# Kernel tuning notes

Measured on AMD Instinct MI355X. Metric: run time of the kernel, lower is better.

The kernel has to match this reference:

```python
import jax, jax.numpy as jnp
import numpy as np

N_NODES = 50000

def _gat_conv(x, src, dst, W, a_src, a_dst, bias, num_nodes, concat, neg_slope=0.2):
    # x: [N, Fin]; W: [Fin, H*C]; a_src/a_dst: [H, C]; src/dst: [E]
    H, C = a_src.shape
    h = (x @ W).reshape(-1, H, C)                      # [N, H, C]
    alpha_s = jnp.einsum('nhc,hc->nh', h, a_src)        # [N, H]
    alpha_d = jnp.einsum('nhc,hc->nh', h, a_dst)        # [N, H]
    e = alpha_s[src] + alpha_d[dst]                     # [E, H]
    e = jax.nn.leaky_relu(e, neg_slope)
    # segment softmax over destination nodes
    m = jax.ops.segment_max(e, dst, num_segments=num_nodes)   # [N, H]
    ex = jnp.exp(e - m[dst])                                   # [E, H]
    denom = jax.ops.segment_sum(ex, dst, num_segments=num_nodes)  # [N, H]
    alpha = ex / denom[dst]                                    # [E, H]
    msg = h[src] * alpha[:, :, None]                            # [E, H, C]
    out = jax.ops.segment_sum(msg, dst, num_segments=num_nodes)  # [N, H, C]
    if concat:
        out = out.reshape(-1, H * C)
    else:
        out = out.mean(axis=1)
    return out + bias

def _add_self_loops(edge_index, num_nodes):
    loop = jnp.arange(num_nodes, dtype=edge_index.dtype)
    src = jnp.concatenate([edge_index[0], loop])
    dst = jnp.concatenate([edge_index[1], loop])
    return src, dst

def setup_inputs() -> dict:
    key = jax.random.key(0)
    ks = jax.random.split(key, 12)
    N, E = N_NODES, 800000
    in_c, hid, out_c, H = 128, 32, 64, 4
    x = jax.random.normal(ks[0], (N, in_c), dtype=jnp.float32)
    edge_index = jax.random.randint(ks[1], (2, E), 0, N, dtype=jnp.int64)
    edge_weight = jax.random.uniform(ks[2], (E,), dtype=jnp.float32)
    s1 = 1.0 / np.sqrt(in_c)
    s2 = 1.0 / np.sqrt(hid * H)
    W1 = jax.random.normal(ks[3], (in_c, H * hid), dtype=jnp.float32) * s1
    a_src1 = jax.random.normal(ks[4], (H, hid), dtype=jnp.float32) * s1
    a_dst1 = jax.random.normal(ks[5], (H, hid), dtype=jnp.float32) * s1
    b1 = jnp.zeros((H * hid,), dtype=jnp.float32)
    W2 = jax.random.normal(ks[6], (H * hid, out_c), dtype=jnp.float32) * s2
    a_src2 = jax.random.normal(ks[7], (1, out_c), dtype=jnp.float32) * s2
    a_dst2 = jax.random.normal(ks[8], (1, out_c), dtype=jnp.float32) * s2
    b2 = jnp.zeros((out_c,), dtype=jnp.float32)
    return {"x": x, "edge_index": edge_index, "edge_weight": edge_weight,
            "W1": W1, "a_src1": a_src1, "a_dst1": a_dst1, "b1": b1,
            "W2": W2, "a_src2": a_src2, "a_dst2": a_dst2, "b2": b2}

def reference(x, edge_index, edge_weight, W1, a_src1, a_dst1, b1, W2, a_src2, a_dst2, b2):
    # PyG GATConv with edge_dim unset ignores edge_weight; self-loops added by default
    N = x.shape[0]
    src, dst = _add_self_loops(edge_index, N)
    h = _gat_conv(x, src, dst, W1, a_src1, a_dst1, b1, N, concat=True)
    h = jax.nn.relu(h)
    out = _gat_conv(h, src, dst, W2, a_src2, a_dst2, b2, N, concat=False)
    return out
```

## Files before the change

kernel.cpp:

```cpp
#include <hip/hip_runtime.h>
#include <hip/hip_fp16.h>
#include <math.h>


#define NEG_SLOPE 0.2f
#define NBLKA 256
#define MAXNB 512
#define LDH 136

typedef _Float16 f16x8 __attribute__((ext_vector_type(8)));
typedef float f32x4 __attribute__((ext_vector_type(4)));

__device__ __forceinline__ float leaky(float v) { return v > 0.f ? v : NEG_SLOPE * v; }

__global__ __launch_bounds__(256) void histc_k(const int* __restrict__ ei, int E, int ET,
                                               int* __restrict__ blkpref, int NB,
                                               const float* __restrict__ W1,
                                               const float* __restrict__ W2,
                                               _Float16* __restrict__ w1t,
                                               _Float16* __restrict__ w2t) {
  __shared__ int lhist[MAXNB];
  int chunk = (ET + NBLKA - 1) / NBLKA;
  int e0 = blockIdx.x * chunk, e1 = min(ET, e0 + chunk);
  for (int b = threadIdx.x; b < NB; b += 256) lhist[b] = 0;
  __syncthreads();
  for (int e = e0 + threadIdx.x; e < e1; e += 256) {
    int d = (e < E) ? ei[E + e] : (e - E);
    atomicAdd(&lhist[d >> 7], 1);
  }
  __syncthreads();
  for (int b = threadIdx.x; b < NB; b += 256)
    blkpref[b * NBLKA + blockIdx.x] = lhist[b];
  if (blockIdx.x == 0) {
    int t = threadIdx.x;
    if (t < 128) {
      union { _Float16 h[8]; uint4 u; } buf;
      for (int k0 = 0; k0 < 128; k0 += 8) {
        #pragma unroll
        for (int u = 0; u < 8; ++u) buf.h[u] = (_Float16)W1[(k0 + u) * 128 + t];
        *(uint4*)&w1t[t * 128 + k0] = buf.u;
      }
    } else if (t < 192) {
      int n = t - 128;
      union { _Float16 h[8]; uint4 u; } buf;
      for (int k0 = 0; k0 < 128; k0 += 8) {
        #pragma unroll
        for (int u = 0; u < 8; ++u) buf.h[u] = (_Float16)W2[(k0 + u) * 64 + n];
        *(uint4*)&w2t[n * 128 + k0] = buf.u;
      }
    }
  }
}

__global__ __launch_bounds__(256) void scan_blk_k(int* __restrict__ blkpref,
                                                  int* __restrict__ bbase) {
  __shared__ int sm[NBLKA];
  int b = blockIdx.x, t = threadIdx.x;
  int v = blkpref[b * NBLKA + t];
  sm[t] = v;
  __syncthreads();
  #pragma unroll
  for (int off = 1; off < NBLKA; off <<= 1) {
    int x = (t >= off) ? sm[t - off] : 0;
    __syncthreads();
    sm[t] += x;
    __syncthreads();
  }
  blkpref[b * NBLKA + t] = sm[t] - v;
  if (t == NBLKA - 1) bbase[b] = sm[t];
}

__global__ __launch_bounds__(512) void scan_bkt_k(int* __restrict__ bbase,
                                                  int* __restrict__ lcnt,
                                                  int* __restrict__ rowptr,
                                                  int NB, int N, int ET) {
  __shared__ int sm[512];
  int t = threadIdx.x;
  int v = (t < NB) ? bbase[t] : 0;
  sm[t] = v;
  __syncthreads();
  #pragma unroll
  for (int off = 1; off < 512; off <<= 1) {
    int x = (t >= off) ? sm[t - off] : 0;
    __syncthreads();
    sm[t] += x;
    __syncthreads();
  }
  int excl = sm[t] - v;
  if (t <= NB) bbase[t] = excl;
  if (t == 0) { lcnt[0] = 0; lcnt[16] = 0; rowptr[N] = ET; }
}

__global__ __launch_bounds__(256) void passA_k(const int* __restrict__ ei, int E, int ET,
                                               const int* __restrict__ bbase,
                                               const int* __restrict__ blkpref,
                                               int* __restrict__ pairs, int NB) {
  __shared__ int lcur[MAXNB];
  int chunk = (ET + NBLKA - 1) / NBLKA;
  int e0 = blockIdx.x * chunk, e1 = min(ET, e0 + chunk);
  for (int b = threadIdx.x; b < NB; b += 256)
    lcur[b] = bbase[b] + blkpref[b * NBLKA + blockIdx.x];
  __syncthreads();
  for (int e = e0 + threadIdx.x; e < e1; e += 256) {
    int s, d;
    if (e < E) { s = ei[e]; d = ei[E + e]; } else { s = d = e - E; }
    int b = d >> 7;
    int pos = atomicAdd(&lcur[b], 1);
    pairs[pos] = ((d & 127) << 17) | s;
  }
}

__global__ __launch_bounds__(256) void passB_k(const int* __restrict__ pairs,
                                               const int* __restrict__ bbase,
                                               int* __restrict__ rowptr,
                                               int* __restrict__ srcs,
                                               int* __restrict__ small_list,
                                               int* __restrict__ big_list,
                                               int* __restrict__ lcnt, int N) {
  __shared__ int ncnt[128], spre[128], lcur[128];
  __shared__ int wcS[2], wcB[2], bS, bB;
  int b = blockIdx.x, t = threadIdx.x;
  int nb0 = b << 7;
  int nn = min(128, N - nb0);
  int e0 = bbase[b], e1 = bbase[b + 1];
  if (t < 128) ncnt[t] = 0;
  __syncthreads();
  for (int r = e0 + t; r < e1; r += 256)
    atomicAdd(&ncnt[pairs[r] >> 17], 1);
  __syncthreads();
  if (t < 128) spre[t] = ncnt[t];
  __syncthreads();
  #pragma unroll
  for (int off = 1; off < 128; off <<= 1) {
    int x = (t < 128 && t >= off) ? spre[t - off] : 0;
    __syncthreads();
    if (t < 128) spre[t] += x;
    __syncthreads();
  }
  if (t < nn) {
    int base = e0 + spre[t] - ncnt[t];
    rowptr[nb0 + t] = base;
    lcur[t] = base;
  }
  __syncthreads();
  for (int r = e0 + t; r < e1; r += 256) {
    int p = pairs[r];
    int pos = atomicAdd(&lcur[p >> 17], 1);
    srcs[pos] = p & 0x1FFFF;
  }
  int lane = t & 63, wv = t >> 6;
  bool valid = (t < nn);
  int deg = valid ? ncnt[t] : 0;
  bool isS = valid && (deg <= 16);
  bool isB = valid && (deg > 16);
  unsigned long long ms = __ballot(isS);
  unsigned long long mb = __ballot(isB);
  if (lane == 0 && wv < 2) { wcS[wv] = __popcll(ms); wcB[wv] = __popcll(mb); }
  __syncthreads();
  if (t == 0) {
    bS = atomicAdd(&lcnt[0],  wcS[0] + wcS[1]);
    bB = atomicAdd(&lcnt[16], wcB[0] + wcB[1]);
  }
  __syncthreads();
  unsigned long long below = (lane == 0) ? 0ull : (~0ull >> (64 - lane));
  int offS = bS + ((wv == 1) ? wcS[0] : 0);
  int offB = bB + ((wv == 1) ? wcB[0] : 0);
  if (isS) small_list[offS + __popcll(ms & below)] = nb0 + t;
  if (isB) big_list[offB + __popcll(mb & below)]   = nb0 + t;
}

__global__ __launch_bounds__(256) void gemm1_k(const float* __restrict__ X,
                                               const _Float16* __restrict__ WT,
                                               const float* __restrict__ aw_s,
                                               const float* __restrict__ aw_d,
                                               __half* __restrict__ Hh,
                                               float* __restrict__ as,
                                               float* __restrict__ ad, int N) {
  __shared__ _Float16 xs[64 * LDH];
  __shared__ _Float16 wt[128 * LDH];
  int t = threadIdx.x;
  int n0 = blockIdx.x * 64;
  for (int i = t; i < 2048; i += 256) {
    int r = i >> 4, c8 = i & 15;
    *(uint4*)&wt[r * LDH + c8 * 8] = ((const uint4*)WT)[i];
  }
  for (int i = t; i < 2048; i += 256) {
    int r = i >> 5, c4 = i & 31;
    int n = n0 + r;
    float4 xv = (n < N) ? ((const float4*)X)[(size_t)n * 32 + c4]
                        : make_float4(0.f, 0.f, 0.f, 0.f);
    __half2 h0 = __floats2half2_rn(xv.x, xv.y);
    __half2 h1 = __floats2half2_rn(xv.z, xv.w);
    uint2 u; u.x = *(unsigned*)&h0; u.y = *(unsigned*)&h1;
    *(uint2*)&xs[r * LDH + c4 * 4] = u;
  }
  __syncthreads();
  int wv = t >> 6, l = t & 63;
  int row16 = l & 15, kg = l >> 4;
  f32x4 acc[8];
  #pragma unroll
  for (int j = 0; j < 8; ++j) acc[j] = (f32x4){0.f, 0.f, 0.f, 0.f};
  #pragma unroll
  for (int kk = 0; kk < 4; ++kk) {
    int kbase = kk * 32 + kg * 8;
    f16x8 afr = *(f16x8*)&xs[(wv * 16 + row16) * LDH + kbase];
    #pragma unroll
    for (int j = 0; j < 8; ++j) {
      f16x8 bfr = *(f16x8*)&wt[(j * 16 + row16) * LDH + kbase];
      acc[j] = __builtin_amdgcn_mfma_f32_16x16x32_f16(afr, bfr, acc[j], 0, 0, 0);
    }
  }
  __syncthreads();
  #pragma unroll
  for (int j = 0; j < 8; ++j) {
    int col = j * 16 + row16;
    #pragma unroll
    for (int r = 0; r < 4; ++r) {
      int row = wv * 16 + kg * 4 + r;
      xs[row * LDH + col] = (_Float16)acc[j][r];
    }
  }
  __syncthreads();
  for (int i = t; i < 1024; i += 256) {
    int r = i >> 4, c8 = i & 15;
    int n = n0 + r;
    if (n < N) ((uint4*)Hh)[(size_t)n * 16 + c8] = *(uint4*)&xs[r * LDH + c8 * 8];
  }
  {
    int r = t >> 2, h = t & 3;
    int n = n0 + r;
    float ps = 0.f, pd = 0.f;
    #pragma unroll
    for (int q = 0; q < 4; ++q) {
      f16x8 hv = *(f16x8*)&xs[r * LDH + h * 32 + q * 8];
      float4 s0 = *(const float4*)&aw_s[h * 32 + q * 8];
      float4 s1 = *(const float4*)&aw_s[h * 32 + q * 8 + 4];
      float4 d0 = *(const float4*)&aw_d[h * 32 + q * 8];
      float4 d1 = *(const float4*)&aw_d[h * 32 + q * 8 + 4];
      ps += (float)hv[0] * s0.x + (float)hv[1] * s0.y + (float)hv[2] * s0.z + (float)hv[3] * s0.w
          + (float)hv[4] * s1.x + (float)hv[5] * s1.y + (float)hv[6] * s1.z + (float)hv[7] * s1.w;
      pd += (float)hv[0] * d0.x + (float)hv[1] * d0.y + (float)hv[2] * d0.z + (float)hv[3] * d0.w
          + (float)hv[4] * d1.x + (float)hv[5] * d1.y + (float)hv[6] * d1.z + (float)hv[7] * d1.w;
    }
    if (n < N) { as[n * 4 + h] = ps; ad[n * 4 + h] = pd; }
  }
}

__global__ __launch_bounds__(256) void gemm2_k(const __half* __restrict__ X,
                                               const _Float16* __restrict__ WT,
                                               const float* __restrict__ aw_s,
                                               const float* __restrict__ aw_d,
                                               __half* __restrict__ Hh,
                                               float* __restrict__ as,
                                               float* __restrict__ ad, int N) {
  __shared__ _Float16 xs[64 * LDH];
  __shared__ _Float16 wt[64 * LDH];
  int t = threadIdx.x;
  int n0 = blockIdx.x * 64;
  for (int i = t; i < 1024; i += 256) {
    int r = i >> 4, c8 = i & 15;
    *(uint4*)&wt[r * LDH + c8 * 8] = ((const uint4*)WT)[i];
  }
  for (int i = t; i < 1024; i += 256) {
    int r = i >> 4, c8 = i & 15;
    int n = n0 + r;
    uint4 v = (n < N) ? ((const uint4*)X)[(size_t)n * 16 + c8] : make_uint4(0, 0, 0, 0);
    *(uint4*)&xs[r * LDH + c8 * 8] = v;
  }
  __syncthreads();
  int wv = t >> 6, l = t & 63;
  int row16 = l & 15, kg = l >> 4;
  f32x4 acc[4];
  #pragma unroll
  for (int j = 0; j < 4; ++j) acc[j] = (f32x4){0.f, 0.f, 0.f, 0.f};
  #pragma unroll
  for (int kk = 0; kk < 4; ++kk) {
    int kbase = kk * 32 + kg * 8;
    f16x8 afr = *(f16x8*)&xs[(wv * 16 + row16) * LDH + kbase];
    #pragma unroll
    for (int j = 0; j < 4; ++j) {
      f16x8 bfr = *(f16x8*)&wt[(j * 16 + row16) * LDH + kbase];
      acc[j] = __builtin_amdgcn_mfma_f32_16x16x32_f16(afr, bfr, acc[j], 0, 0, 0);
    }
  }
  __syncthreads();
  #pragma unroll
  for (int j = 0; j < 4; ++j) {
    int col = j * 16 + row16;
    #pragma unroll
    for (int r = 0; r < 4; ++r) {
      int row = wv * 16 + kg * 4 + r;
      xs[row * LDH + col] = (_Float16)acc[j][r];
    }
  }
  __syncthreads();
  for (int i = t; i < 512; i += 256) {
    int r = i >> 3, c8 = i & 7;
    int n = n0 + r;
    if (n < N) ((uint4*)Hh)[(size_t)n * 8 + c8] = *(uint4*)&xs[r * LDH + c8 * 8];
  }
  {
    int r = t >> 2, q = t & 3;
    int n = n0 + r;
    float ps = 0.f, pd = 0.f;
    #pragma unroll
    for (int qq = 0; qq < 2; ++qq) {
      f16x8 hv = *(f16x8*)&xs[r * LDH + q * 16 + qq * 8];
      float4 s0 = *(const float4*)&aw_s[q * 16 + qq * 8];
      float4 s1 = *(const float4*)&aw_s[q * 16 + qq * 8 + 4];
      float4 d0 = *(const float4*)&aw_d[q * 16 + qq * 8];
      float4 d1 = *(const float4*)&aw_d[q * 16 + qq * 8 + 4];
      ps += (float)hv[0] * s0.x + (float)hv[1] * s0.y + (float)hv[2] * s0.z + (float)hv[3] * s0.w
          + (float)hv[4] * s1.x + (float)hv[5] * s1.y + (float)hv[6] * s1.z + (float)hv[7] * s1.w;
      pd += (float)hv[0] * d0.x + (float)hv[1] * d0.y + (float)hv[2] * d0.z + (float)hv[3] * d0.w
          + (float)hv[4] * d1.x + (float)hv[5] * d1.y + (float)hv[6] * d1.z + (float)hv[7] * d1.w;
    }
    ps += __shfl_xor(ps, 1); ps += __shfl_xor(ps, 2);
    pd += __shfl_xor(pd, 1); pd += __shfl_xor(pd, 2);
    if (q == 0 && n < N) { as[n] = ps; ad[n] = pd; }
  }
}

__device__ __forceinline__ void load8h(const __half* p, float* f) {
  uint4 hv = *(const uint4*)p;
  float2 f0 = __half22float2(*(const __half2*)&hv.x);
  float2 f1 = __half22float2(*(const __half2*)&hv.y);
  float2 f2 = __half22float2(*(const __half2*)&hv.z);
  float2 f3 = __half22float2(*(const __half2*)&hv.w);
  f[0] = f0.x; f[1] = f0.y; f[2] = f1.x; f[3] = f1.y;
  f[4] = f2.x; f[5] = f2.y; f[6] = f3.x; f[7] = f3.y;
}

__global__ __launch_bounds__(256) void agg1_k(const int* __restrict__ rowptr,
                                              const int* __restrict__ srcs,
                                              const float* __restrict__ as,
                                              const float* __restrict__ ad,
                                              const __half* __restrict__ Hm,
                                              const float* __restrict__ bias,
                                              __half* __restrict__ out,
                                              const int* __restrict__ small_list,
                                              const int* __restrict__ big_list,
                                              const int* __restrict__ lcnt, int SB) {
  if (blockIdx.x < (unsigned)SB) {
    __shared__ float al_sm[16][17][4];
    __shared__ int   sr_sm[16][16];
    int g  = threadIdx.x >> 4;
    int gl = threadIdx.x & 15;
    int gidx = blockIdx.x * 16 + g;
    if (gidx >= lcnt[0]) return;
    int n = small_list[gidx];
    int r0 = rowptr[n];
    int deg = rowptr[n + 1] - r0;
    float4 adn = *(const float4*)&ad[n * 4];

    float e0 = -INFINITY, e1 = -INFINITY, e2 = -INFINITY, e3 = -INFINITY;
    int s = 0;
    if (gl < deg) {
      s = srcs[r0 + gl];
      float4 av = *(const float4*)&as[s * 4];
      e0 = leaky(av.x + adn.x); e1 = leaky(av.y + adn.y);
      e2 = leaky(av.z + adn.z); e3 = leaky(av.w + adn.w);
    }
    sr_sm[g][gl] = s;
    float m0 = e0, m1 = e1, m2 = e2, m3 = e3;
    #pragma unroll
    for (int off = 8; off > 0; off >>= 1) {
      m0 = fmaxf(m0, __shfl_xor(m0, off, 16)); m1 = fmaxf(m1, __shfl_xor(m1, off, 16));
      m2 = fmaxf(m2, __shfl_xor(m2, off, 16)); m3 = fmaxf(m3, __shfl_xor(m3, off, 16));
    }
    float sc0 = (gl < deg) ? __expf(e0 - m0) : 0.f;
    float sc1 = (gl < deg) ? __expf(e1 - m1) : 0.f;
    float sc2 = (gl < deg) ? __expf(e2 - m2) : 0.f;
    float sc3 = (gl < deg) ? __expf(e3 - m3) : 0.f;
    float s0 = sc0, s1 = sc1, s2 = sc2, s3 = sc3;
    #pragma unroll
    for (int off = 8; off > 0; off >>= 1) {
      s0 += __shfl_xor(s0, off, 16); s1 += __shfl_xor(s1, off, 16);
      s2 += __shfl_xor(s2, off, 16); s3 += __shfl_xor(s3, off, 16);
    }
    *(float4*)&al_sm[g][gl][0] =
        make_float4(sc0 / s0, sc1 / s1, sc2 / s2, sc3 / s3);

    int h = gl >> 2;
    int cbase = gl * 8;
    float a0 = 0.f, a1 = 0.f, a2 = 0.f, a3 = 0.f,
          a4 = 0.f, a5 = 0.f, a6 = 0.f, a7 = 0.f;
    for (int j = 0; j < deg; j += 4) {
      #pragma unroll
      for (int u = 0; u < 4; ++u) {
        int idx = j + u;
        bool vU = idx < deg;
        int jj = vU ? idx : 0;
        int   sU  = sr_sm[g][jj];
        float alU = vU ? al_sm[g][jj][h] : 0.f;
        float f[8];
        load8h(&Hm[(size_t)sU * 128 + cbase], f);
        a0 += f[0] * alU; a1 += f[1] * alU; a2 += f[2] * alU; a3 += f[3] * alU;
        a4 += f[4] * alU; a5 += f[5] * alU; a6 += f[6] * alU; a7 += f[7] * alU;
      }
    }
    float4 b0 = *(const float4*)&bias[cbase];
    float4 b1 = *(const float4*)&bias[cbase + 4];
    __half2* dst = (__half2*)&out[(size_t)n * 128 + cbase];
    dst[0] = __floats2half2_rn(fmaxf(a0 + b0.x, 0.f), fmaxf(a1 + b0.y, 0.f));
    dst[1] = __floats2half2_rn(fmaxf(a2 + b0.z, 0.f), fmaxf(a3 + b0.w, 0.f));
    dst[2] = __floats2half2_rn(fmaxf(a4 + b1.x, 0.f), fmaxf(a5 + b1.y, 0.f));
    dst[3] = __floats2half2_rn(fmaxf(a6 + b1.z, 0.f), fmaxf(a7 + b1.w, 0.f));
    return;
  }
  __shared__ float al_sm[4][64][4];
  __shared__ int   sr_sm[4][64];
  int wv = threadIdx.x >> 6, lane = threadIdx.x & 63;
  int widx = (blockIdx.x - SB) * 4 + wv;
  if (widx >= lcnt[16]) return;
  int n = big_list[widx];
  int r0 = rowptr[n], r1 = rowptr[n + 1];
  int deg = r1 - r0;
  int grp = lane >> 4, gl = lane & 15, h = gl >> 2;
  int cbase = gl * 8;
  float4 adn = *(const float4*)&ad[n * 4];

  float a0 = 0.f, a1 = 0.f, a2 = 0.f, a3 = 0.f,
        a4 = 0.f, a5 = 0.f, a6 = 0.f, a7 = 0.f;

  if (deg <= 64) {
    float e0 = -INFINITY, e1 = -INFINITY, e2 = -INFINITY, e3 = -INFINITY;
    int s = 0;
    if (lane < deg) {
      s = srcs[r0 + lane];
      float4 av = *(const float4*)&as[s * 4];
      e0 = leaky(av.x + adn.x); e1 = leaky(av.y + adn.y);
      e2 = leaky(av.z + adn.z); e3 = leaky(av.w + adn.w);
    }
    sr_sm[wv][lane] = s;
    float m0 = e0, m1 = e1, m2 = e2, m3 = e3;
    #pragma unroll
    for (int off = 32; off > 0; off >>= 1) {
      m0 = fmaxf(m0, __shfl_xor(m0, off)); m1 = fmaxf(m1, __shfl_xor(m1, off));
      m2 = fmaxf(m2, __shfl_xor(m2, off)); m3 = fmaxf(m3, __shfl_xor(m3, off));
    }
    float sc0 = (lane < deg) ? __expf(e0 - m0) : 0.f;
    float sc1 = (lane < deg) ? __expf(e1 - m1) : 0.f;
    float sc2 = (lane < deg) ? __expf(e2 - m2) : 0.f;
    float sc3 = (lane < deg) ? __expf(e3 - m3) : 0.f;
    float s0 = sc0, s1 = sc1, s2 = sc2, s3 = sc3;
    #pragma unroll
    for (int off = 32; off > 0; off >>= 1) {
      s0 += __shfl_xor(s0, off); s1 += __shfl_xor(s1, off);
      s2 += __shfl_xor(s2, off); s3 += __shfl_xor(s3, off);
    }
    *(float4*)&al_sm[wv][lane][0] =
        make_float4(sc0 / s0, sc1 / s1, sc2 / s2, sc3 / s3);

    for (int base = 0; base < deg; base += 16) {
      #pragma unroll
      for (int u = 0; u < 4; ++u) {
        int idx = base + grp * 4 + u;
        bool vU = idx < deg;
        int jj = vU ? idx : 0;
        int   sU  = sr_sm[wv][jj];
        float alU = vU ? al_sm[wv][jj][h] : 0.f;
        float f[8];
        load8h(&Hm[(size_t)sU * 128 + cbase], f);
        a0 += f[0] * alU; a1 += f[1] * alU; a2 += f[2] * alU; a3 += f[3] * alU;
        a4 += f[4] * alU; a5 += f[5] * alU; a6 += f[6] * alU; a7 += f[7] * alU;
      }
    }
  } else {
    float m0 = -INFINITY, m1 = -INFINITY, m2 = -INFINITY, m3 = -INFINITY;
    for (int r = r0 + lane; r < r1; r += 64) {
      int s = srcs[r];
      float4 av = *(const float4*)&as[s * 4];
      m0 = fmaxf(m0, leaky(av.x + adn.x)); m1 = fmaxf(m1, leaky(av.y + adn.y));
      m2 = fmaxf(m2, leaky(av.z + adn.z)); m3 = fmaxf(m3, leaky(av.w + adn.w));
    }
    #pragma unroll
    for (int off = 32; off > 0; off >>= 1) {
      m0 = fmaxf(m0, __shfl_xor(m0, off)); m1 = fmaxf(m1, __shfl_xor(m1, off));
      m2 = fmaxf(m2, __shfl_xor(m2, off)); m3 = fmaxf(m3, __shfl_xor(m3, off));
    }
    float s0 = 0.f, s1 = 0.f, s2 = 0.f, s3 = 0.f;
    for (int r = r0 + lane; r < r1; r += 64) {
      int s = srcs[r];
      float4 av = *(const float4*)&as[s * 4];
      s0 += __expf(leaky(av.x + adn.x) - m0); s1 += __expf(leaky(av.y + adn.y) - m1);
      s2 += __expf(leaky(av.z + adn.z) - m2); s3 += __expf(leaky(av.w + adn.w) - m3);
    }
    #pragma unroll
    for (int off = 32; off > 0; off >>= 1) {
      s0 += __shfl_xor(s0, off); s1 += __shfl_xor(s1, off);
      s2 += __shfl_xor(s2, off); s3 += __shfl_xor(s3, off);
    }
    float mhh = (h == 0) ? m0 : (h == 1) ? m1 : (h == 2) ? m2 : m3;
    float inv = 1.f / ((h == 0) ? s0 : (h == 1) ? s1 : (h == 2) ? s2 : s3);
    float adh = (h == 0) ? adn.x : (h == 1) ? adn.y : (h == 2) ? adn.z : adn.w;
    for (int r = r0; r < r1; r += 8) {
      int rA = r + grp, rB = rA + 4;
      bool vA = rA < r1, vB = rB < r1;
      int sA = srcs[vA ? rA : r0];
      int sB = srcs[vB ? rB : r0];
      float avA = as[sA * 4 + h], avB = as[sB * 4 + h];
      float alA = vA ? (__expf(leaky(avA + adh) - mhh) * inv) : 0.f;
      float alB = vB ? (__expf(leaky(avB + adh) - mhh) * inv) : 0.f;
      float fA[8], fB[8];
      load8h(&Hm[(size_t)sA * 128 + cbase], fA);
      load8h(&Hm[(size_t)sB * 128 + cbase], fB);
      a0 += fA[0] * alA + fB[0] * alB; a1 += fA[1] * alA + fB[1] * alB;
      a2 += fA[2] * alA + fB[2] * alB; a3 += fA[3] * alA + fB[3] * alB;
      a4 += fA[4] * alA + fB[4] * alB; a5 += fA[5] * alA + fB[5] * alB;
      a6 += fA[6] * alA + fB[6] * alB; a7 += fA[7] * alA + fB[7] * alB;
    }
  }
  a0 += __shfl_xor(a0, 16); a0 += __shfl_xor(a0, 32);
  a1 += __shfl_xor(a1, 16); a1 += __shfl_xor(a1, 32);
  a2 += __shfl_xor(a2, 16); a2 += __shfl_xor(a2, 32);
  a3 += __shfl_xor(a3, 16); a3 += __shfl_xor(a3, 32);
  a4 += __shfl_xor(a4, 16); a4 += __shfl_xor(a4, 32);
  a5 += __shfl_xor(a5, 16); a5 += __shfl_xor(a5, 32);
  a6 += __shfl_xor(a6, 16); a6 += __shfl_xor(a6, 32);
  a7 += __shfl_xor(a7, 16); a7 += __shfl_xor(a7, 32);
  if (grp == 0) {
    float4 b0 = *(const float4*)&bias[cbase];
    float4 b1 = *(const float4*)&bias[cbase + 4];
    __half2* dst = (__half2*)&out[(size_t)n * 128 + cbase];
    dst[0] = __floats2half2_rn(fmaxf(a0 + b0.x, 0.f), fmaxf(a1 + b0.y, 0.f));
    dst[1] = __floats2half2_rn(fmaxf(a2 + b0.z, 0.f), fmaxf(a3 + b0.w, 0.f));
    dst[2] = __floats2half2_rn(fmaxf(a4 + b1.x, 0.f), fmaxf(a5 + b1.y, 0.f));
    dst[3] = __floats2half2_rn(fmaxf(a6 + b1.z, 0.f), fmaxf(a7 + b1.w, 0.f));
  }
}

__global__ __launch_bounds__(256) void agg2_k(const int* __restrict__ rowptr,
                                              const int* __restrict__ srcs,
                                              const float* __restrict__ as,
                                              const float* __restrict__ ad,
                                              const __half* __restrict__ Hm,
                                              const float* __restrict__ bias,
                                              float* __restrict__ out,
                                              const int* __restrict__ small_list,
                                              const int* __restrict__ big_list,
                                              const int* __restrict__ lcnt, int SB) {
  if (blockIdx.x < (unsigned)SB) {
    __shared__ float al_sm[16][17];
    __shared__ int   sr_sm[16][16];
    int g  = threadIdx.x >> 4;
    int gl = threadIdx.x & 15;
    int gidx = blockIdx.x * 16 + g;
    if (gidx >= lcnt[0]) return;
    int n = small_list[gidx];
    int r0 = rowptr[n];
    int deg = rowptr[n + 1] - r0;
    float adn = ad[n];

    float e = -INFINITY;
    int s = 0;
    if (gl < deg) { s = srcs[r0 + gl]; e = leaky(as[s] + adn); }
    sr_sm[g][gl] = s;
    float m = e;
    #pragma unroll
    for (int off = 8; off > 0; off >>= 1) m = fmaxf(m, __shfl_xor(m, off, 16));
    float sc = (gl < deg) ? __expf(e - m) : 0.f;
    float ssum = sc;
    #pragma unroll
    for (int off = 8; off > 0; off >>= 1) ssum += __shfl_xor(ssum, off, 16);
    al_sm[g][gl] = sc / ssum;

    int cbase = gl * 4;
    float a0 = 0.f, a1 = 0.f, a2 = 0.f, a3 = 0.f;
    for (int j = 0; j < deg; j += 4) {
      #pragma unroll
      for (int u = 0; u < 4; ++u) {
        int idx = j + u;
        bool vU = idx < deg;
        int jj = vU ? idx : 0;
        int   sU  = sr_sm[g][jj];
        float alU = vU ? al_sm[g][jj] : 0.f;
        uint2 hv = *(const uint2*)&Hm[(size_t)sU * 64 + cbase];
        float2 f0 = __half22float2(*(const __half2*)&hv.x);
        float2 f1 = __half22float2(*(const __half2*)&hv.y);
        a0 += f0.x * alU; a1 += f0.y * alU; a2 += f1.x * alU; a3 += f1.y * alU;
      }
    }
    float4 bv = *(const float4*)&bias[cbase];
    float4 o;
    o.x = a0 + bv.x; o.y = a1 + bv.y; o.z = a2 + bv.z; o.w = a3 + bv.w;
    *(float4*)&out[(size_t)n * 64 + cbase] = o;
    return;
  }
  __shared__ float al_sm[4][64];
  __shared__ int   sr_sm[4][64];
  int wv = threadIdx.x >> 6, lane = threadIdx.x & 63;
  int widx = (blockIdx.x - SB) * 4 + wv;
  if (widx >= lcnt[16]) return;
  int n = big_list[widx];
  int r0 = rowptr[n], r1 = rowptr[n + 1];
  int deg = r1 - r0;
  int grp = lane >> 4, gl = lane & 15;
  int cbase = gl * 4;
  float adn = ad[n];

  float a0 = 0.f, a1 = 0.f, a2 = 0.f, a3 = 0.f;

  if (deg <= 64) {
    float e = -INFINITY;
    int s = 0;
    if (lane < deg) { s = srcs[r0 + lane]; e = leaky(as[s] + adn); }
    sr_sm[wv][lane] = s;
    float m = e;
    #pragma unroll
    for (int off = 32; off > 0; off >>= 1) m = fmaxf(m, __shfl_xor(m, off));
    float sc = (lane < deg) ? __expf(e - m) : 0.f;
    float ssum = sc;
    #pragma unroll
    for (int off = 32; off > 0; off >>= 1) ssum += __shfl_xor(ssum, off);
    al_sm[wv][lane] = sc / ssum;

    for (int base = 0; base < deg; base += 16) {
      #pragma unroll
      for (int u = 0; u < 4; ++u) {
        int idx = base + grp * 4 + u;
        bool vU = idx < deg;
        int jj = vU ? idx : 0;
        int   sU  = sr_sm[wv][jj];
        float alU = vU ? al_sm[wv][jj] : 0.f;
        uint2 hv = *(const uint2*)&Hm[(size_t)sU * 64 + cbase];
        float2 f0 = __half22float2(*(const __half2*)&hv.x);
        float2 f1 = __half22float2(*(const __half2*)&hv.y);
        a0 += f0.x * alU; a1 += f0.y * alU; a2 += f1.x * alU; a3 += f1.y * alU;
      }
    }
  } else {
    float mh = -INFINITY;
    for (int r = r0 + lane; r < r1; r += 64)
      mh = fmaxf(mh, leaky(as[srcs[r]] + adn));
    #pragma unroll
    for (int off = 32; off > 0; off >>= 1) mh = fmaxf(mh, __shfl_xor(mh, off));
    float ssum = 0.f;
    for (int r = r0 + lane; r < r1; r += 64)
      ssum += __expf(leaky(as[srcs[r]] + adn) - mh);
    #pragma unroll
    for (int off = 32; off > 0; off >>= 1) ssum += __shfl_xor(ssum, off);
    float inv = 1.f / ssum;
    for (int r = r0; r < r1; r += 8) {
      int rA = r + grp, rB = rA + 4;
      bool vA = rA < r1, vB = rB < r1;
      int sA = srcs[vA ? rA : r0];
      int sB = srcs[vB ? rB : r0];
      float alA = vA ? (__expf(leaky(as[sA] + adn) - mh) * inv) : 0.f;
      float alB = vB ? (__expf(leaky(as[sB] + adn) - mh) * inv) : 0.f;
      uint2 hvA = *(const uint2*)&Hm[(size_t)sA * 64 + cbase];
      uint2 hvB = *(const uint2*)&Hm[(size_t)sB * 64 + cbase];
      float2 fA0 = __half22float2(*(const __half2*)&hvA.x);
      float2 fA1 = __half22float2(*(const __half2*)&hvA.y);
      float2 fB0 = __half22float2(*(const __half2*)&hvB.x);
      float2 fB1 = __half22float2(*(const __half2*)&hvB.y);
      a0 += fA0.x * alA + fB0.x * alB; a1 += fA0.y * alA + fB0.y * alB;
      a2 += fA1.x * alA + fB1.x * alB; a3 += fA1.y * alA + fB1.y * alB;
    }
  }
  a0 += __shfl_xor(a0, 16); a0 += __shfl_xor(a0, 32);
  a1 += __shfl_xor(a1, 16); a1 += __shfl_xor(a1, 32);
  a2 += __shfl_xor(a2, 16); a2 += __shfl_xor(a2, 32);
  a3 += __shfl_xor(a3, 16); a3 += __shfl_xor(a3, 32);
  if (grp == 0) {
    float4 bv = *(const float4*)&bias[cbase];
    float4 o;
    o.x = a0 + bv.x; o.y = a1 + bv.y; o.z = a2 + bv.z; o.w = a3 + bv.w;
    *(float4*)&out[(size_t)n * 64 + cbase] = o;
  }
}

extern "C" void kernel_launch(void* const* d_in, const int* in_sizes, int n_in,
                              void* d_out, int out_size, void* d_ws, size_t ws_size,
                              hipStream_t stream) {
  const float* x   = (const float*)d_in[0];
  const int*   ei  = (const int*)d_in[1];
  const float* W1  = (const float*)d_in[3];
  const float* aS1 = (const float*)d_in[4];
  const float* aD1 = (const float*)d_in[5];
  const float* b1  = (const float*)d_in[6];
  const float* W2  = (const float*)d_in[7];
  const float* aS2 = (const float*)d_in[8];
  const float* aD2 = (const float*)d_in[9];
  const float* b2  = (const float*)d_in[10];

  const int N  = in_sizes[0] / 128;
  const int E  = in_sizes[2];
  const int ET = E + N;
  const int NB = (N + 127) >> 7;

  float* ws    = (float*)d_ws;
  __half* h1h  = (__half*)ws;
  __half* o1h  = (__half*)(ws + (size_t)N * 64);
  float* as1   = ws + (size_t)N * 128;
  float* ad1   = as1  + (size_t)4 * N;
  float* as2   = ad1  + (size_t)4 * N;
  float* ad2   = as2  + (size_t)N;
  int*   lcnt    = (int*)(ad2 + (size_t)N);
  int*   rowptr  = lcnt + 32;
  int*   bbase   = rowptr + N + 1;
  int*   blkpref = bbase + NB + 1;
  int*   small_list = blkpref + NB * NBLKA;
  int*   big_list   = small_list + N;
  int*   srcs   = big_list + N;
  _Float16* w1t = (_Float16*)(srcs + ET);
  _Float16* w2t = w1t + 128 * 128;
  int*   pairs  = (int*)ws;
  __half* h2h  = h1h;
  float* out  = (float*)d_out;

  const int gb = (N + 63) / 64;
  const int sb = (N + 15) / 16;
  const int bb = (N + 3) / 4;

  histc_k<<<NBLKA, 256, 0, stream>>>(ei, E, ET, blkpref, NB, W1, W2, w1t, w2t);
  scan_blk_k<<<NB, 256, 0, stream>>>(blkpref, bbase);
  scan_bkt_k<<<1, 512, 0, stream>>>(bbase, lcnt, rowptr, NB, N, ET);
  passA_k<<<NBLKA, 256, 0, stream>>>(ei, E, ET, bbase, blkpref, pairs, NB);
  passB_k<<<NB, 256, 0, stream>>>(pairs, bbase, rowptr, srcs,
                                  small_list, big_list, lcnt, N);

  gemm1_k<<<gb, 256, 0, stream>>>(x, w1t, aS1, aD1, h1h, as1, ad1, N);
  agg1_k<<<sb + bb, 256, 0, stream>>>(rowptr, srcs, as1, ad1, h1h, b1, o1h,
                                      small_list, big_list, lcnt, sb);

  gemm2_k<<<gb, 256, 0, stream>>>(o1h, w2t, aS2, aD2, h2h, as2, ad2, N);
  agg2_k<<<sb + bb, 256, 0, stream>>>(rowptr, srcs, as2, ad2, h2h, b2, out,
                                      small_list, big_list, lcnt, sb);
}
```

Baseline: 216.4 us.

## Fuse layer-1 GEMM into histogram kernel via block-index dispatch

```diff
diff --git a/kernel.cpp b/kernel.cpp
--- a/kernel.cpp
+++ b/kernel.cpp
@@ -10,45 +10,116 @@
 
 typedef _Float16 f16x8 __attribute__((ext_vector_type(8)));
 typedef float f32x4 __attribute__((ext_vector_type(4)));
+typedef unsigned int u32x4 __attribute__((ext_vector_type(4)));
 
 __device__ __forceinline__ float leaky(float v) { return v > 0.f ? v : NEG_SLOPE * v; }
 
-__global__ __launch_bounds__(256) void histc_k(const int* __restrict__ ei, int E, int ET,
-                                               int* __restrict__ blkpref, int NB,
-                                               const float* __restrict__ W1,
-                                               const float* __restrict__ W2,
-                                               _Float16* __restrict__ w1t,
-                                               _Float16* __restrict__ w2t) {
-  __shared__ int lhist[MAXNB];
-  int chunk = (ET + NBLKA - 1) / NBLKA;
-  int e0 = blockIdx.x * chunk, e1 = min(ET, e0 + chunk);
-  for (int b = threadIdx.x; b < NB; b += 256) lhist[b] = 0;
-  __syncthreads();
-  for (int e = e0 + threadIdx.x; e < e1; e += 256) {
-    int d = (e < E) ? ei[E + e] : (e - E);
-    atomicAdd(&lhist[d >> 7], 1);
-  }
-  __syncthreads();
-  for (int b = threadIdx.x; b < NB; b += 256)
-    blkpref[b * NBLKA + blockIdx.x] = lhist[b];
-  if (blockIdx.x == 0) {
-    int t = threadIdx.x;
-    if (t < 128) {
-      union { _Float16 h[8]; uint4 u; } buf;
+__global__ __launch_bounds__(256) void histc_gemm1_k(const int* __restrict__ ei, int E, int ET,
+                                                     int* __restrict__ blkpref, int NB,
+                                                     const float* __restrict__ W1,
+                                                     const float* __restrict__ W2,
+                                                     _Float16* __restrict__ w2t,
+                                                     const float* __restrict__ X,
+                                                     const float* __restrict__ aw_s,
+                                                     const float* __restrict__ aw_d,
+                                                     __half* __restrict__ Hh,
+                                                     float* __restrict__ as,
+                                                     float* __restrict__ ad, int N) {
+  __shared__ float smemf[13056];
+  int t = threadIdx.x;
+  if (blockIdx.x < NBLKA) {
+    int* lhist = (int*)smemf;
+    int chunk = (ET + NBLKA - 1) / NBLKA;
+    int e0 = blockIdx.x * chunk, e1 = min(ET, e0 + chunk);
+    for (int b = t; b < NB; b += 256) lhist[b] = 0;
+    __syncthreads();
+    for (int e = e0 + t; e < e1; e += 256) {
+      int d = (e < E) ? ei[E + e] : (e - E);
+      atomicAdd(&lhist[d >> 7], 1);
+    }
+    __syncthreads();
+    for (int b = t; b < NB; b += 256)
+      blkpref[b * NBLKA + blockIdx.x] = lhist[b];
+    if (blockIdx.x == 0 && t < 64) {
+      union { _Float16 h[8]; u32x4 u; } buf;
       for (int k0 = 0; k0 < 128; k0 += 8) {
         #pragma unroll
-        for (int u = 0; u < 8; ++u) buf.h[u] = (_Float16)W1[(k0 + u) * 128 + t];
-        *(uint4*)&w1t[t * 128 + k0] = buf.u;
+        for (int u = 0; u < 8; ++u) buf.h[u] = (_Float16)W2[(k0 + u) * 64 + t];
+        *(u32x4*)&w2t[t * 128 + k0] = buf.u;
       }
-    } else if (t < 192) {
-      int n = t - 128;
-      union { _Float16 h[8]; uint4 u; } buf;
-      for (int k0 = 0; k0 < 128; k0 += 8) {
-        #pragma unroll
-        for (int u = 0; u < 8; ++u) buf.h[u] = (_Float16)W2[(k0 + u) * 64 + n];
-        *(uint4*)&w2t[n * 128 + k0] = buf.u;
-      }
-    }
+    }
+    return;
+  }
+  _Float16* xs = (_Float16*)smemf;
+  _Float16* wt = xs + 64 * LDH;
+  int n0 = (blockIdx.x - NBLKA) * 64;
+  for (int i = t; i < 4096; i += 256) {
+    int k = i >> 5, n4 = (i & 31) * 4;
+    float4 wv = *(const float4*)&W1[k * 128 + n4];
+    wt[(n4 + 0) * LDH + k] = (_Float16)wv.x;
+    wt[(n4 + 1) * LDH + k] = (_Float16)wv.y;
+    wt[(n4 + 2) * LDH + k] = (_Float16)wv.z;
+    wt[(n4 + 3) * LDH + k] = (_Float16)wv.w;
+  }
+  for (int i = t; i < 2048; i += 256) {
+    int r = i >> 5, c4 = i & 31;
+    int n = n0 + r;
+    float4 xv = (n < N) ? *(const float4*)&X[(size_t)n * 128 + c4 * 4]
+                        : make_float4(0.f, 0.f, 0.f, 0.f);
+    __half2 h0 = __floats2half2_rn(xv.x, xv.y);
+    __half2 h1 = __floats2half2_rn(xv.z, xv.w);
+    uint2 u; u.x = *(unsigned*)&h0; u.y = *(unsigned*)&h1;
+    *(uint2*)&xs[r * LDH + c4 * 4] = u;
+  }
+  __syncthreads();
+  int wv = t >> 6, l = t & 63;
+  int row16 = l & 15, kg = l >> 4;
+  f32x4 acc[8];
+  #pragma unroll
+  for (int j = 0; j < 8; ++j) acc[j] = (f32x4){0.f, 0.f, 0.f, 0.f};
+  #pragma unroll
+  for (int kk = 0; kk < 4; ++kk) {
+    int kbase = kk * 32 + kg * 8;
+    f16x8 afr = *(f16x8*)&xs[(wv * 16 + row16) * LDH + kbase];
+    #pragma unroll
+    for (int j = 0; j < 8; ++j) {
+      f16x8 bfr = *(f16x8*)&wt[(j * 16 + row16) * LDH + kbase];
+      acc[j] = __builtin_amdgcn_mfma_f32_16x16x32_f16(afr, bfr, acc[j], 0, 0, 0);
+    }
+  }
+  __syncthreads();
+  #pragma unroll
+  for (int j = 0; j < 8; ++j) {
+    int col = j * 16 + row16;
+    #pragma unroll
+    for (int r = 0; r < 4; ++r) {
+      int row = wv * 16 + kg * 4 + r;
+      xs[row * LDH + col] = (_Float16)acc[j][r];
+    }
+  }
+  __syncthreads();
+  for (int i = t; i < 1024; i += 256) {
+    int r = i >> 4, c8 = i & 15;
+    int n = n0 + r;
+    if (n < N) ((u32x4*)Hh)[(size_t)n * 16 + c8] = *(u32x4*)&xs[r * LDH + c8 * 8];
+  }
+  {
+    int r = t >> 2, h = t & 3;
+    int n = n0 + r;
+    float ps = 0.f, pd = 0.f;
+    #pragma unroll
+    for (int q = 0; q < 4; ++q) {
+      f16x8 hv = *(f16x8*)&xs[r * LDH + h * 32 + q * 8];
+      float4 s0 = *(const float4*)&aw_s[h * 32 + q * 8];
+      float4 s1 = *(const float4*)&aw_s[h * 32 + q * 8 + 4];
+      float4 d0 = *(const float4*)&aw_d[h * 32 + q * 8];
+      float4 d1 = *(const float4*)&aw_d[h * 32 + q * 8 + 4];
+      ps += (float)hv[0] * s0.x + (float)hv[1] * s0.y + (float)hv[2] * s0.z + (float)hv[3] * s0.w
+          + (float)hv[4] * s1.x + (float)hv[5] * s1.y + (float)hv[6] * s1.z + (float)hv[7] * s1.w;
+      pd += (float)hv[0] * d0.x + (float)hv[1] * d0.y + (float)hv[2] * d0.z + (float)hv[3] * d0.w
+          + (float)hv[4] * d1.x + (float)hv[5] * d1.y + (float)hv[6] * d1.z + (float)hv[7] * d1.w;
+    }
+    if (n < N) { as[n * 4 + h] = ps; ad[n * 4 + h] = pd; }
   }
 }
 
@@ -169,83 +240,6 @@
   if (isB) big_list[offB + __popcll(mb & below)]   = nb0 + t;
 }
 
-__global__ __launch_bounds__(256) void gemm1_k(const float* __restrict__ X,
-                                               const _Float16* __restrict__ WT,
-                                               const float* __restrict__ aw_s,
-                                               const float* __restrict__ aw_d,
-                                               __half* __restrict__ Hh,
-                                               float* __restrict__ as,
-                                               float* __restrict__ ad, int N) {
-  __shared__ _Float16 xs[64 * LDH];
-  __shared__ _Float16 wt[128 * LDH];
-  int t = threadIdx.x;
-  int n0 = blockIdx.x * 64;
-  for (int i = t; i < 2048; i += 256) {
-    int r = i >> 4, c8 = i & 15;
-    *(uint4*)&wt[r * LDH + c8 * 8] = ((const uint4*)WT)[i];
-  }
-  for (int i = t; i < 2048; i += 256) {
-    int r = i >> 5, c4 = i & 31;
-    int n = n0 + r;
-    float4 xv = (n < N) ? ((const float4*)X)[(size_t)n * 32 + c4]
-                        : make_float4(0.f, 0.f, 0.f, 0.f);
-    __half2 h0 = __floats2half2_rn(xv.x, xv.y);
-    __half2 h1 = __floats2half2_rn(xv.z, xv.w);
-    uint2 u; u.x = *(unsigned*)&h0; u.y = *(unsigned*)&h1;
-    *(uint2*)&xs[r * LDH + c4 * 4] = u;
-  }
-  __syncthreads();
-  int wv = t >> 6, l = t & 63;
-  int row16 = l & 15, kg = l >> 4;
-  f32x4 acc[8];
-  #pragma unroll
-  for (int j = 0; j < 8; ++j) acc[j] = (f32x4){0.f, 0.f, 0.f, 0.f};
-  #pragma unroll
-  for (int kk = 0; kk < 4; ++kk) {
-    int kbase = kk * 32 + kg * 8;
-    f16x8 afr = *(f16x8*)&xs[(wv * 16 + row16) * LDH + kbase];
-    #pragma unroll
-    for (int j = 0; j < 8; ++j) {
-      f16x8 bfr = *(f16x8*)&wt[(j * 16 + row16) * LDH + kbase];
-      acc[j] = __builtin_amdgcn_mfma_f32_16x16x32_f16(afr, bfr, acc[j], 0, 0, 0);
-    }
-  }
-  __syncthreads();
-  #pragma unroll
-  for (int j = 0; j < 8; ++j) {
-    int col = j * 16 + row16;
-    #pragma unroll
-    for (int r = 0; r < 4; ++r) {
-      int row = wv * 16 + kg * 4 + r;
-      xs[row * LDH + col] = (_Float16)acc[j][r];
-    }
-  }
-  __syncthreads();
-  for (int i = t; i < 1024; i += 256) {
-    int r = i >> 4, c8 = i & 15;
-    int n = n0 + r;
-    if (n < N) ((uint4*)Hh)[(size_t)n * 16 + c8] = *(uint4*)&xs[r * LDH + c8 * 8];
-  }
-  {
-    int r = t >> 2, h = t & 3;
-    int n = n0 + r;
-    float ps = 0.f, pd = 0.f;
-    #pragma unroll
-    for (int q = 0; q < 4; ++q) {
-      f16x8 hv = *(f16x8*)&xs[r * LDH + h * 32 + q * 8];
-      float4 s0 = *(const float4*)&aw_s[h * 32 + q * 8];
-      float4 s1 = *(const float4*)&aw_s[h * 32 + q * 8 + 4];
-      float4 d0 = *(const float4*)&aw_d[h * 32 + q * 8];
-      float4 d1 = *(const float4*)&aw_d[h * 32 + q * 8 + 4];
-      ps += (float)hv[0] * s0.x + (float)hv[1] * s0.y + (float)hv[2] * s0.z + (float)hv[3] * s0.w
-          + (float)hv[4] * s1.x + (float)hv[5] * s1.y + (float)hv[6] * s1.z + (float)hv[7] * s1.w;
-      pd += (float)hv[0] * d0.x + (float)hv[1] * d0.y + (float)hv[2] * d0.z + (float)hv[3] * d0.w
-          + (float)hv[4] * d1.x + (float)hv[5] * d1.y + (float)hv[6] * d1.z + (float)hv[7] * d1.w;
-    }
-    if (n < N) { as[n * 4 + h] = ps; ad[n * 4 + h] = pd; }
-  }
-}
-
 __global__ __launch_bounds__(256) void gemm2_k(const __half* __restrict__ X,
                                                const _Float16* __restrict__ WT,
                                                const float* __restrict__ aw_s,
@@ -259,13 +253,13 @@
   int n0 = blockIdx.x * 64;
   for (int i = t; i < 1024; i += 256) {
     int r = i >> 4, c8 = i & 15;
-    *(uint4*)&wt[r * LDH + c8 * 8] = ((const uint4*)WT)[i];
+    *(u32x4*)&wt[r * LDH + c8 * 8] = ((const u32x4*)WT)[i];
   }
   for (int i = t; i < 1024; i += 256) {
     int r = i >> 4, c8 = i & 15;
     int n = n0 + r;
-    uint4 v = (n < N) ? ((const uint4*)X)[(size_t)n * 16 + c8] : make_uint4(0, 0, 0, 0);
-    *(uint4*)&xs[r * LDH + c8 * 8] = v;
+    u32x4 v = (n < N) ? ((const u32x4*)X)[(size_t)n * 16 + c8] : (u32x4){0, 0, 0, 0};
+    *(u32x4*)&xs[r * LDH + c8 * 8] = v;
   }
   __syncthreads();
   int wv = t >> 6, l = t & 63;
@@ -297,7 +291,7 @@
   for (int i = t; i < 512; i += 256) {
     int r = i >> 3, c8 = i & 7;
     int n = n0 + r;
-    if (n < N) ((uint4*)Hh)[(size_t)n * 8 + c8] = *(uint4*)&xs[r * LDH + c8 * 8];
+    if (n < N) ((u32x4*)Hh)[(size_t)n * 8 + c8] = *(u32x4*)&xs[r * LDH + c8 * 8];
   }
   {
     int r = t >> 2, q = t & 3;
@@ -703,9 +697,9 @@
   int*   small_list = blkpref + NB * NBLKA;
   int*   big_list   = small_list + N;
   int*   srcs   = big_list + N;
-  _Float16* w1t = (_Float16*)(srcs + ET);
-  _Float16* w2t = w1t + 128 * 128;
+  _Float16* w2t = (_Float16*)(srcs + ET);
   int*   pairs  = (int*)ws;
+  int*   pairs_sep = (int*)(w2t + 64 * 128);
   __half* h2h  = h1h;
   float* out  = (float*)d_out;
 
@@ -713,14 +707,14 @@
   const int sb = (N + 15) / 16;
   const int bb = (N + 3) / 4;
 
-  histc_k<<<NBLKA, 256, 0, stream>>>(ei, E, ET, blkpref, NB, W1, W2, w1t, w2t);
+  histc_gemm1_k<<<NBLKA + gb, 256, 0, stream>>>(ei, E, ET, blkpref, NB, W1, W2, w2t,
+                                                x, aS1, aD1, h1h, as1, ad1, N);
   scan_blk_k<<<NB, 256, 0, stream>>>(blkpref, bbase);
   scan_bkt_k<<<1, 512, 0, stream>>>(bbase, lcnt, rowptr, NB, N, ET);
-  passA_k<<<NBLKA, 256, 0, stream>>>(ei, E, ET, bbase, blkpref, pairs, NB);
-  passB_k<<<NB, 256, 0, stream>>>(pairs, bbase, rowptr, srcs,
+  passA_k<<<NBLKA, 256, 0, stream>>>(ei, E, ET, bbase, blkpref, pairs_sep, NB);
+  passB_k<<<NB, 256, 0, stream>>>(pairs_sep, bbase, rowptr, srcs,
                                   small_list, big_list, lcnt, N);
 
-  gemm1_k<<<gb, 256, 0, stream>>>(x, w1t, aS1, aD1, h1h, as1, ad1, N);
   agg1_k<<<sb + bb, 256, 0, stream>>>(rowptr, srcs, as1, ad1, h1h, b1, o1h,
                                       small_list, big_list, lcnt, sb);
 
```

New measurement: 215.5 us. No clear change (-0.4%).
